# Performance work log

Hardware: AMD Instinct MI355X
Metric: run time of the kernel (lower is better)

Reference implementation:

```python
import jax, jax.numpy as jnp
import numpy as np
from itertools import combinations_with_replacement

LATENT_DIM = 16
N_PARAMS = 2
N_VARS = LATENT_DIM + N_PARAMS  # 18
POLY_ORDER = 3
BATCH = 131072

# Static exponent index tables: for each degree d, an [n_terms_d, d] array of
# variable indices (combinations with replacement), matching a sympy-style
# polynomial library [1, x_i, x_i*x_j, x_i*x_j*x_k, ...].
IDX = [np.array(list(combinations_with_replacement(range(N_VARS), d)), dtype=np.int32)
       for d in range(1, POLY_ORDER + 1)]
P = 1 + sum(a.shape[0] for a in IDX)  # 1330 library terms


def setup_inputs() -> dict:
    key = jax.random.key(0)
    k1, k2, k3 = jax.random.split(key, 3)
    z = jax.random.normal(k1, (BATCH, LATENT_DIM), dtype=jnp.float32)
    betas = jax.random.normal(k2, (BATCH, N_PARAMS), dtype=jnp.float32)
    big_xi = jax.random.normal(k3, (P, N_VARS), dtype=jnp.float32) * 0.1
    mask = jnp.ones((P, N_VARS), dtype=jnp.float32)
    return {"z": z, "betas": betas, "big_xi": big_xi, "mask": mask}


def _theta(x):
    # x: [B, N_VARS] -> theta: [B, P]
    cols = [jnp.ones((x.shape[0], 1), dtype=x.dtype)]  # constant term
    for idx in IDX:
        acc = x[:, idx[:, 0]]                # [B, n_terms_d]
        for k in range(1, idx.shape[1]):     # loop over degree (<= POLY_ORDER)
            acc = acc * x[:, idx[:, k]]
        cols.append(acc)
    return jnp.concatenate(cols, axis=1)


def reference(z, betas, big_xi, mask):
    x = jnp.concatenate([z, betas], axis=1)  # [B, N_VARS]
    theta = _theta(x)                        # [B, P]
    return theta @ (big_xi * mask)           # [B, N_VARS]
```

## Files before the change

### kernel.cpp

```cpp
#include <hip/hip_runtime.h>
#include <hip/hip_bf16.h>
#include <utility>


constexpr int NVARS   = 18;
constexpr int NOUT    = 18;
constexpr int NROWS   = 131072;
constexpr int NCHUNKS = 43;
constexpr int NSLOTS  = NCHUNKS * 8;

constexpr int CH_STRIDE = 304;
constexpr int WF2_SHORTS = 86 * CH_STRIDE;
constexpr int LDS_SHORTS = 32768;

typedef __attribute__((ext_vector_type(8)))  short short8;
typedef __attribute__((ext_vector_type(16))) float f32x16;

struct T3 { int a, b, c; };

constexpr int rho1(int v) {
    if (v < 16)  return (v & ~3) | ((v + 1) & 3);
    if (v == 16) return 17;
    if (v == 17) return 16;
    return v;
}
constexpr int rho2v(int v) { return rho1(rho1(v)); }

constexpr T3 sort3(int u0, int u1, int u2) {
    int t = 0;
    if (u0 > u1) { t = u0; u0 = u1; u1 = t; }
    if (u1 > u2) { t = u1; u1 = u2; u2 = t; }
    if (u0 > u1) { t = u0; u0 = u1; u1 = t; }
    return T3{u0, u1, u2};
}
constexpr T3 rho3(T3 t) { return sort3(rho1(t.a), rho1(t.b), rho1(t.c)); }

constexpr bool t3_less(T3 x, T3 y) {
    if (x.a != y.a) return x.a < y.a;
    if (x.b != y.b) return x.b < y.b;
    return x.c < y.c;
}
constexpr bool t3_eq(T3 x, T3 y) { return x.a == y.a && x.b == y.b && x.c == y.c; }

constexpr int rank_of(T3 t) {
    int deg = (t.a < 18) + (t.b < 18) + (t.c < 18);
    if (deg == 0) return 0;
    if (deg == 1) return 1 + t.a;
    if (deg == 2) {
        int r = 19;
        for (int a = 0; a < t.a; ++a) r += 18 - a;
        return r + (t.b - t.a);
    }
    int r = 190;
    for (int a = 0; a < t.a; ++a) { int n = 18 - a; r += n * (n + 1) / 2; }
    for (int b = t.a; b < t.b; ++b) r += 18 - b;
    return r + (t.c - t.b);
}

struct RepTables {
    signed char va[NSLOTS], vb[NSLOTS], vc[NSLOTS];
    short p[4][NSLOTS];
    int count;
};

constexpr void consider(RepTables& R, int& s, T3 t) {
    T3 im[4] = {t, T3{0, 0, 0}, T3{0, 0, 0}, T3{0, 0, 0}};
    im[1] = rho3(im[0]);
    im[2] = rho3(im[1]);
    im[3] = rho3(im[2]);
    for (int g = 1; g < 4; ++g)
        if (t3_less(im[g], t)) return;
    R.va[s] = (signed char)t.a; R.vb[s] = (signed char)t.b; R.vc[s] = (signed char)t.c;
    for (int g = 0; g < 4; ++g) {
        bool dup = false;
        for (int h = 0; h < g; ++h)
            if (t3_eq(im[h], im[g])) dup = true;
        R.p[g][s] = dup ? (short)-1 : (short)rank_of(im[g]);
    }
    ++s;
}

constexpr RepTables make_tables() {
    RepTables R{};
    int s = 0;
    consider(R, s, T3{18, 18, 18});
    for (int a = 0; a < NVARS; ++a) consider(R, s, T3{a, 18, 18});
    for (int a = 0; a < NVARS; ++a)
        for (int b = a; b < NVARS; ++b) consider(R, s, T3{a, b, 18});
    for (int a = 0; a < NVARS; ++a)
        for (int b = a; b < NVARS; ++b)
            for (int c = b; c < NVARS; ++c) consider(R, s, T3{a, b, c});
    R.count = s;
    for (; s < NSLOTS; ++s) {
        R.va[s] = 19; R.vb[s] = 19; R.vc[s] = 19;
        for (int g = 0; g < 4; ++g) R.p[g][s] = -1;
    }
    return R;
}

constexpr RepTables h_tab = make_tables();
static_assert(h_tab.count == 342, "orbit enumeration must give 342 rep slots");
__device__ const RepTables d_tab = make_tables();

__device__ __align__(16) short g_wf2[WF2_SHORTS];


#if __has_builtin(__builtin_amdgcn_cvt_pk_bf16_f32)
typedef __bf16 bf16x2 __attribute__((ext_vector_type(2)));
__device__ __forceinline__ unsigned pack2(float f0, float f1) {
    bf16x2 r = __builtin_amdgcn_cvt_pk_bf16_f32(f0, f1);
    return __builtin_bit_cast(unsigned, r);
}
#else
__device__ __forceinline__ unsigned pack2(float f0, float f1) {
    unsigned u0 = __float_as_uint(f0) + 0x8000u;
    unsigned u1 = __float_as_uint(f1) + 0x8000u;
    return __builtin_amdgcn_perm(u1, u0, 0x07060302u);
}
#endif


template <int S>
__device__ __forceinline__ float term_val(const float (&x)[NVARS]) {
    constexpr int a = h_tab.va[S], b = h_tab.vb[S], c = h_tab.vc[S];
    if constexpr (a >= 19)      return 0.0f;
    else if constexpr (a == 18) return 1.0f;
    else if constexpr (b == 18) return x[a];
    else if constexpr (c == 18) return x[a] * x[b];
    else                        return x[a] * x[b] * x[c];
}

union AFrag { unsigned u[4]; short8 v; };

template <int S, int... J>
__device__ __forceinline__ void pack8(const float (&x)[NVARS], AFrag& af,
                                      std::integer_sequence<int, J...>) {
    ((af.u[J] = pack2(term_val<S + 2 * J>(x), term_val<S + 2 * J + 1>(x))), ...);
}

template <int CI>
__device__ __forceinline__ void kstep32(const float (&x)[NVARS],
                                        const short* pB, f32x16& acc) {
    constexpr int S = (CI < 43 ? CI : CI - 43) * 8;
    AFrag af;
    pack8<S>(x, af, std::make_integer_sequence<int, 4>{});
    short8 b = *(const short8*)(pB + CI * CH_STRIDE);
    acc = __builtin_amdgcn_mfma_f32_32x32x16_bf16(af.v, b, acc, 0, 0, 0);
}

template <int BASE, int... CI>
__device__ __forceinline__ void kloop32(const float (&x)[NVARS],
                                        const short* pB, f32x16& acc,
                                        std::integer_sequence<int, CI...>) {
    (kstep32<BASE + CI>(x, pB, acc), ...);
}

__device__ __forceinline__ void load_x(const float* __restrict__ z,
                                       const float* __restrict__ betas,
                                       int arow, bool s1, float (&x)[NVARS]) {
    float x0[NVARS];
    const float4* z4 = (const float4*)(z + (size_t)arow * 16);
    float4 v0 = z4[0], v1 = z4[1], v2 = z4[2], v3 = z4[3];
    x0[0]  = v0.x; x0[1]  = v0.y; x0[2]  = v0.z; x0[3]  = v0.w;
    x0[4]  = v1.x; x0[5]  = v1.y; x0[6]  = v1.z; x0[7]  = v1.w;
    x0[8]  = v2.x; x0[9]  = v2.y; x0[10] = v2.z; x0[11] = v2.w;
    x0[12] = v3.x; x0[13] = v3.y; x0[14] = v3.z; x0[15] = v3.w;
    const float2 b2 = *(const float2*)(betas + (size_t)arow * 2);
    x0[16] = b2.x; x0[17] = b2.y;
#pragma unroll
    for (int v = 0; v < NVARS; ++v) x[v] = s1 ? x0[rho1(v)] : x0[v];
}

__global__ __launch_bounds__(512, 4) void vindy_mfma(const float* __restrict__ z,
                                                     const float* __restrict__ betas,
                                                     float* __restrict__ out) {
    __shared__ __align__(16) short ldsW[LDS_SHORTS];

    {
        const float4* src = (const float4*)g_wf2;
        float4* dst = (float4*)ldsW;
        for (int i = threadIdx.x; i < WF2_SHORTS / 8; i += 512) dst[i] = src[i];
    }
    __syncthreads();

    const int lane = threadIdx.x & 63;
    const int wave = threadIdx.x >> 6;
    const int h    = lane >> 5;
    const int col  = lane & 31;
    const int row0 = blockIdx.x * 256 + wave * 32;

    float x1[NVARS];
    load_x(z, betas, row0 + col, h != 0, x1);

    const int col_eff = (col < NOUT) ? col : NOUT;
    const short* pB = ldsW + h * 152 + col_eff * 8;

    f32x16 acc;
#pragma unroll
    for (int i = 0; i < 16; ++i) acc[i] = 0.0f;

    kloop32<0>(x1, pB, acc, std::make_integer_sequence<int, 43>{});

    float x2[NVARS];
#pragma unroll
    for (int v = 0; v < NVARS; ++v) x2[v] = x1[rho2v(v)];

    kloop32<43>(x2, pB, acc, std::make_integer_sequence<int, 43>{});

    if (col < NOUT) {
#pragma unroll
        for (int q = 0; q < 4; ++q) {
#pragma unroll
            for (int r = 0; r < 4; ++r) {
                int row = r + 8 * q + 4 * h;
                out[(size_t)(row0 + row) * NOUT + col] = acc[q * 4 + r];
            }
        }
    }
}


__global__ void prep_wfrag(const float* __restrict__ xi, const float* __restrict__ mask) {
    int i = blockIdx.x * blockDim.x + threadIdx.x;
    if (i >= WF2_SHORTS) return;
    int c  = i / CH_STRIDE;
    int r  = i - c * CH_STRIDE;
    int h  = r / 152;
    int r2 = r - h * 152;
    int col = r2 >> 3, j = r2 & 7;
    float v = 0.0f;
    if (col < NOUT) {
        int g = (c < 43 ? 0 : 2) + h;
        int s = (c < 43 ? c : c - 43) * 8 + j;
        int p = d_tab.p[g][s];
        if (p >= 0) v = xi[p * NOUT + col] * mask[p * NOUT + col];
    }
    g_wf2[i] = __builtin_bit_cast(short, __float2bfloat16(v));
}

extern "C" void kernel_launch(void* const* d_in, const int* in_sizes, int n_in,
                              void* d_out, int out_size, void* d_ws, size_t ws_size,
                              hipStream_t stream) {
    const float* z     = (const float*)d_in[0];
    const float* betas = (const float*)d_in[1];
    const float* xi    = (const float*)d_in[2];
    const float* mask  = (const float*)d_in[3];
    float* out = (float*)d_out;
    (void)d_ws; (void)ws_size;

    prep_wfrag<<<(WF2_SHORTS + 255) / 256, 256, 0, stream>>>(xi, mask);
    vindy_mfma<<<NROWS / 256, 512, 0, stream>>>(z, betas, out);
}
```

Baseline: 86.04 us.

## Split K-loop across wave pairs and reduce partial accumulators through LDS

Each 32-row tile is now handled by two waves, and each wave runs one of the two orbit-group K halves (43 MFMA steps instead of 86). Blocks grow to 1024 threads. The partial 32x32 accumulators are exchanged and summed through LDS, and each wave writes half of the output rows. This shortens the serial MFMA chain per wave and adds parallelism, at the cost of extra syncthreads, an LDS reduction step, and twice as many x loads and permutations per row.

```diff
diff --git a/kernel.cpp b/kernel.cpp
--- a/kernel.cpp
+++ b/kernel.cpp
@@ -11,9 +11,9 @@
 
 constexpr int CH_STRIDE = 304;
 constexpr int WF2_SHORTS = 86 * CH_STRIDE;
-constexpr int LDS_SHORTS = 32768;
 
 typedef __attribute__((ext_vector_type(8)))  short short8;
+typedef __attribute__((ext_vector_type(4)))  float f32x4v;
 typedef __attribute__((ext_vector_type(16))) float f32x16;
 
 struct T3 { int a, b, c; };
@@ -141,23 +141,22 @@
 template <int CI>
 __device__ __forceinline__ void kstep32(const float (&x)[NVARS],
                                         const short* pB, f32x16& acc) {
-    constexpr int S = (CI < 43 ? CI : CI - 43) * 8;
     AFrag af;
-    pack8<S>(x, af, std::make_integer_sequence<int, 4>{});
+    pack8<CI * 8>(x, af, std::make_integer_sequence<int, 4>{});
     short8 b = *(const short8*)(pB + CI * CH_STRIDE);
     acc = __builtin_amdgcn_mfma_f32_32x32x16_bf16(af.v, b, acc, 0, 0, 0);
 }
 
-template <int BASE, int... CI>
+template <int... CI>
 __device__ __forceinline__ void kloop32(const float (&x)[NVARS],
                                         const short* pB, f32x16& acc,
                                         std::integer_sequence<int, CI...>) {
-    (kstep32<BASE + CI>(x, pB, acc), ...);
+    (kstep32<CI>(x, pB, acc), ...);
 }
 
 __device__ __forceinline__ void load_x(const float* __restrict__ z,
                                        const float* __restrict__ betas,
-                                       int arow, bool s1, float (&x)[NVARS]) {
+                                       int arow, bool s1, bool s2, float (&x)[NVARS]) {
     float x0[NVARS];
     const float4* z4 = (const float4*)(z + (size_t)arow * 16);
     float4 v0 = z4[0], v1 = z4[1], v2 = z4[2], v3 = z4[3];
@@ -167,49 +166,64 @@
     x0[12] = v3.x; x0[13] = v3.y; x0[14] = v3.z; x0[15] = v3.w;
     const float2 b2 = *(const float2*)(betas + (size_t)arow * 2);
     x0[16] = b2.x; x0[17] = b2.y;
-#pragma unroll
-    for (int v = 0; v < NVARS; ++v) x[v] = s1 ? x0[rho1(v)] : x0[v];
-}
-
-__global__ __launch_bounds__(512, 4) void vindy_mfma(const float* __restrict__ z,
-                                                     const float* __restrict__ betas,
-                                                     float* __restrict__ out) {
-    __shared__ __align__(16) short ldsW[LDS_SHORTS];
+    float y[NVARS];
+#pragma unroll
+    for (int v = 0; v < NVARS; ++v) y[v] = s1 ? x0[rho1(v)] : x0[v];
+#pragma unroll
+    for (int v = 0; v < NVARS; ++v) x[v] = s2 ? y[rho2v(v)] : y[v];
+}
+
+__global__ __launch_bounds__(1024, 8) void vindy_mfma(const float* __restrict__ z,
+                                                      const float* __restrict__ betas,
+                                                      float* __restrict__ out) {
+    __shared__ __align__(16) short ldsW[WF2_SHORTS];
 
     {
         const float4* src = (const float4*)g_wf2;
         float4* dst = (float4*)ldsW;
-        for (int i = threadIdx.x; i < WF2_SHORTS / 8; i += 512) dst[i] = src[i];
+        for (int i = threadIdx.x; i < WF2_SHORTS / 8; i += 1024) dst[i] = src[i];
     }
     __syncthreads();
 
-    const int lane = threadIdx.x & 63;
-    const int wave = threadIdx.x >> 6;
-    const int h    = lane >> 5;
-    const int col  = lane & 31;
-    const int row0 = blockIdx.x * 256 + wave * 32;
-
-    float x1[NVARS];
-    load_x(z, betas, row0 + col, h != 0, x1);
+    const int lane  = threadIdx.x & 63;
+    const int wave  = threadIdx.x >> 6;
+    const int pair  = wave >> 1;
+    const int phase = wave & 1;
+    const int h     = lane >> 5;
+    const int col   = lane & 31;
+    const int row0  = blockIdx.x * 256 + pair * 32;
+
+    const int g = h + 2 * phase;
+    float x[NVARS];
+    load_x(z, betas, row0 + col, (g & 1) != 0, (g & 2) != 0, x);
 
     const int col_eff = (col < NOUT) ? col : NOUT;
-    const short* pB = ldsW + h * 152 + col_eff * 8;
+    const short* pB = ldsW + phase * (NCHUNKS * CH_STRIDE) + h * 152 + col_eff * 8;
 
     f32x16 acc;
 #pragma unroll
     for (int i = 0; i < 16; ++i) acc[i] = 0.0f;
 
-    kloop32<0>(x1, pB, acc, std::make_integer_sequence<int, 43>{});
-
-    float x2[NVARS];
-#pragma unroll
-    for (int v = 0; v < NVARS; ++v) x2[v] = x1[rho2v(v)];
-
-    kloop32<43>(x2, pB, acc, std::make_integer_sequence<int, 43>{});
+    kloop32(x, pB, acc, std::make_integer_sequence<int, NCHUNKS>{});
+
+    __syncthreads();
+    float* red = (float*)ldsW;
+    {
+        float4* my = (float4*)(red + ((size_t)(pair * 2 + phase) * 64 + lane) * 8);
+        const int src0 = phase ? 0 : 8;
+        my[0] = float4{acc[src0 + 0], acc[src0 + 1], acc[src0 + 2], acc[src0 + 3]};
+        my[1] = float4{acc[src0 + 4], acc[src0 + 5], acc[src0 + 6], acc[src0 + 7]};
+    }
+    __syncthreads();
+    const float* pr = red + ((size_t)(pair * 2 + (1 - phase)) * 64 + lane) * 8;
+    const int dst0 = phase ? 8 : 0;
+#pragma unroll
+    for (int i = 0; i < 8; ++i) acc[dst0 + i] += pr[i];
 
     if (col < NOUT) {
 #pragma unroll
-        for (int q = 0; q < 4; ++q) {
+        for (int qq = 0; qq < 2; ++qq) {
+            const int q = 2 * phase + qq;
 #pragma unroll
             for (int r = 0; r < 4; ++r) {
                 int row = r + 8 * q + 4 * h;
@@ -249,5 +263,5 @@
     (void)d_ws; (void)ws_size;
 
     prep_wfrag<<<(WF2_SHORTS + 255) / 256, 256, 0, stream>>>(xi, mask);
-    vindy_mfma<<<NROWS / 256, 512, 0, stream>>>(z, betas, out);
-}
+    vindy_mfma<<<NROWS / 256, 1024, 0, stream>>>(z, betas, out);
+}
```

After: 114.1 us. 1.33x slower.

## Split symmetry-orbit phases across block pairs and combine with atomics

Applied to the files above, without the earlier changes.

Each block now handles only one half of the orbit group (phase 0 or 1), loading half of the weight fragment table into LDS and running 43 MFMA steps instead of 86. The grid doubles, and the two partial results per row are summed with float atomic adds into an output zeroed by a memset. The smaller LDS footprint allows a higher occupancy hint (8 blocks per CU) and more parallelism. In exchange it adds a memset, atomic traffic on the output, duplicated loads of x, and an order-dependent floating-point sum.

```diff
diff --git a/kernel.cpp b/kernel.cpp
--- a/kernel.cpp
+++ b/kernel.cpp
@@ -9,9 +9,9 @@
 constexpr int NCHUNKS = 43;
 constexpr int NSLOTS  = NCHUNKS * 8;
 
-constexpr int CH_STRIDE = 304;
-constexpr int WF2_SHORTS = 86 * CH_STRIDE;
-constexpr int LDS_SHORTS = 32768;
+constexpr int CH_STRIDE  = 304;
+constexpr int PH_SHORTS  = NCHUNKS * CH_STRIDE;
+constexpr int WF2_SHORTS = 2 * PH_SHORTS;
 
 typedef __attribute__((ext_vector_type(8)))  short short8;
 typedef __attribute__((ext_vector_type(16))) float f32x16;
@@ -141,23 +141,22 @@
 template <int CI>
 __device__ __forceinline__ void kstep32(const float (&x)[NVARS],
                                         const short* pB, f32x16& acc) {
-    constexpr int S = (CI < 43 ? CI : CI - 43) * 8;
     AFrag af;
-    pack8<S>(x, af, std::make_integer_sequence<int, 4>{});
+    pack8<CI * 8>(x, af, std::make_integer_sequence<int, 4>{});
     short8 b = *(const short8*)(pB + CI * CH_STRIDE);
     acc = __builtin_amdgcn_mfma_f32_32x32x16_bf16(af.v, b, acc, 0, 0, 0);
 }
 
-template <int BASE, int... CI>
+template <int... CI>
 __device__ __forceinline__ void kloop32(const float (&x)[NVARS],
                                         const short* pB, f32x16& acc,
                                         std::integer_sequence<int, CI...>) {
-    (kstep32<BASE + CI>(x, pB, acc), ...);
+    (kstep32<CI>(x, pB, acc), ...);
 }
 
 __device__ __forceinline__ void load_x(const float* __restrict__ z,
                                        const float* __restrict__ betas,
-                                       int arow, bool s1, float (&x)[NVARS]) {
+                                       int arow, bool s1, bool s2, float (&x)[NVARS]) {
     float x0[NVARS];
     const float4* z4 = (const float4*)(z + (size_t)arow * 16);
     float4 v0 = z4[0], v1 = z4[1], v2 = z4[2], v3 = z4[3];
@@ -167,19 +166,25 @@
     x0[12] = v3.x; x0[13] = v3.y; x0[14] = v3.z; x0[15] = v3.w;
     const float2 b2 = *(const float2*)(betas + (size_t)arow * 2);
     x0[16] = b2.x; x0[17] = b2.y;
-#pragma unroll
-    for (int v = 0; v < NVARS; ++v) x[v] = s1 ? x0[rho1(v)] : x0[v];
-}
-
-__global__ __launch_bounds__(512, 4) void vindy_mfma(const float* __restrict__ z,
+    float y[NVARS];
+#pragma unroll
+    for (int v = 0; v < NVARS; ++v) y[v] = s1 ? x0[rho1(v)] : x0[v];
+#pragma unroll
+    for (int v = 0; v < NVARS; ++v) x[v] = s2 ? y[rho2v(v)] : y[v];
+}
+
+__global__ __launch_bounds__(512, 8) void vindy_mfma(const float* __restrict__ z,
                                                      const float* __restrict__ betas,
                                                      float* __restrict__ out) {
-    __shared__ __align__(16) short ldsW[LDS_SHORTS];
+    __shared__ __align__(16) short ldsW[PH_SHORTS];
+
+    const int phase = blockIdx.x & 1;
+    const int row0b = (blockIdx.x >> 1) * 256;
 
     {
-        const float4* src = (const float4*)g_wf2;
+        const float4* src = (const float4*)(g_wf2 + phase * PH_SHORTS);
         float4* dst = (float4*)ldsW;
-        for (int i = threadIdx.x; i < WF2_SHORTS / 8; i += 512) dst[i] = src[i];
+        for (int i = threadIdx.x; i < PH_SHORTS / 8; i += 512) dst[i] = src[i];
     }
     __syncthreads();
 
@@ -187,10 +192,11 @@
     const int wave = threadIdx.x >> 6;
     const int h    = lane >> 5;
     const int col  = lane & 31;
-    const int row0 = blockIdx.x * 256 + wave * 32;
-
-    float x1[NVARS];
-    load_x(z, betas, row0 + col, h != 0, x1);
+    const int row0 = row0b + wave * 32;
+
+    const int g = h + 2 * phase;
+    float x[NVARS];
+    load_x(z, betas, row0 + col, (g & 1) != 0, (g & 2) != 0, x);
 
     const int col_eff = (col < NOUT) ? col : NOUT;
     const short* pB = ldsW + h * 152 + col_eff * 8;
@@ -199,21 +205,20 @@
 #pragma unroll
     for (int i = 0; i < 16; ++i) acc[i] = 0.0f;
 
-    kloop32<0>(x1, pB, acc, std::make_integer_sequence<int, 43>{});
-
-    float x2[NVARS];
-#pragma unroll
-    for (int v = 0; v < NVARS; ++v) x2[v] = x1[rho2v(v)];
-
-    kloop32<43>(x2, pB, acc, std::make_integer_sequence<int, 43>{});
+    kloop32(x, pB, acc, std::make_integer_sequence<int, NCHUNKS>{});
 
     if (col < NOUT) {
+        float* obase = out + (size_t)row0 * NOUT + col;
 #pragma unroll
         for (int q = 0; q < 4; ++q) {
 #pragma unroll
             for (int r = 0; r < 4; ++r) {
                 int row = r + 8 * q + 4 * h;
-                out[(size_t)(row0 + row) * NOUT + col] = acc[q * 4 + r];
+#if defined(__HIP_DEVICE_COMPILE__)
+                unsafeAtomicAdd(obase + (size_t)row * NOUT, acc[q * 4 + r]);
+#else
+                atomicAdd(obase + (size_t)row * NOUT, acc[q * 4 + r]);
+#endif
             }
         }
     }
@@ -248,6 +253,7 @@
     float* out = (float*)d_out;
     (void)d_ws; (void)ws_size;
 
+    hipMemsetAsync(out, 0, (size_t)out_size, stream);
     prep_wfrag<<<(WF2_SHORTS + 255) / 256, 256, 0, stream>>>(xi, mask);
-    vindy_mfma<<<NROWS / 256, 512, 0, stream>>>(z, betas, out);
-}
+    vindy_mfma<<<NROWS / 128, 512, 0, stream>>>(z, betas, out);
+}
```

Result: slower. 114.4 us (+32.9%).
